# Performance work log

Measured on AMD Instinct MI355X. Metric: run time of the kernel, lower is better.

The kernel has to match this reference:

```python
import jax, jax.numpy as jnp
import numpy as np

B, N, H, E = 16, 512, 8, 128  # batch, nodes, heads, per-head/embed dim
NEG = -1000000000.0


def _xavier(key, shape):
    fan_out, fan_in = shape
    lim = float(np.sqrt(6.0 / (fan_in + fan_out)))
    return jax.random.uniform(key, shape, jnp.float32, -lim, lim)


def setup_inputs() -> dict:
    key = jax.random.key(0)
    ks = jax.random.split(key, 8)
    x = jax.random.normal(ks[0], (B, N, E), jnp.float32)
    dist = jax.random.normal(ks[1], (B, N, N), jnp.float32)
    mask = (jax.random.uniform(ks[2], (B, N)) > 0.2).astype(jnp.float32)
    Wq = _xavier(ks[3], (H * E, E)); bq = jnp.zeros((H * E,), jnp.float32)
    Wk = _xavier(ks[4], (H * E, E)); bk = jnp.zeros((H * E,), jnp.float32)
    Wv = _xavier(ks[5], (H * E, E)); bv = jnp.zeros((H * E,), jnp.float32)
    Wo = _xavier(ks[6], (E, H * E)); bo = jnp.zeros((E,), jnp.float32)
    return dict(x=x, dist=dist, mask=mask, Wq=Wq, bq=bq, Wk=Wk, bk=bk,
                Wv=Wv, bv=bv, Wo=Wo, bo=bo)


def reference(x, dist, mask, Wq, bq, Wk, bk, Wv, bv, Wo, bo):
    b, n, e = x.shape
    h = Wq.shape[0] // e
    scale = e ** (-0.5)
    # projections -> [b, h, n, e]
    q = (x @ Wq.T + bq).reshape(b, n, h, e).transpose(0, 2, 1, 3)
    k = (x @ Wk.T + bk).reshape(b, n, h, e).transpose(0, 2, 1, 3)
    v = (x @ Wv.T + bv).reshape(b, n, h, e).transpose(0, 2, 1, 3)
    # encoder_mask: zero out padded nodes in q, k, v
    m = mask[:, None, :, None]  # [b,1,n,1]
    q = q * m
    k = k * m
    v = v * m
    # scaled scores + per-graph distance bias broadcast over heads
    a = jnp.einsum('bhqe,bhke->bhqk', q * scale, k) + dist[:, None]
    # pairwise attention mask (outer product of node mask)
    am = (mask[:, :, None] * mask[:, None, :])[:, None]  # [b,1,n,n]
    a = jnp.where(am == 0, NEG, a)
    a = jax.nn.softmax(a, axis=-1)
    a = jnp.where(am == 0, 0.0, a)
    # dropout p=0 -> identity
    y = jnp.einsum('bhqk,bhke->bhqe', a, v)
    y = y.transpose(0, 2, 1, 3).reshape(b, n, h * e)
    y = y @ Wo.T + bo
    y = y * mask[:, :, None]
    return y
```

## Files before the change

### kernel.cpp

```cpp
#include <hip/hip_runtime.h>
#include <math.h>

#define BB 16
#define NN 512
#define HH 8
#define EE 128
#define HE 1024
#define QSCALE 0.08838834764831845f
#define NEGV -1000000000.0f

typedef short bf16x8 __attribute__((ext_vector_type(8)));
typedef float f32x4 __attribute__((ext_vector_type(4)));
typedef unsigned u32x4 __attribute__((ext_vector_type(4)));

__device__ __forceinline__ void split2(float v, unsigned short &hi, unsigned short &lo) {
    union { float f; unsigned u; } a; a.f = v;
    const unsigned r = (a.u + 0x7FFFu + ((a.u >> 16) & 1u)) >> 16;
    hi = (unsigned short)r;
    union { unsigned u; float f; } hf; hf.u = r << 16;
    const float res = v - hf.f;
    union { float f; unsigned u; } c; c.f = res;
    const unsigned r2 = (c.u + 0x7FFFu + ((c.u >> 16) & 1u)) >> 16;
    lo = (unsigned short)r2;
}

__device__ __forceinline__ void gload16(const void* g, void* l) {
    __builtin_amdgcn_global_load_lds(
        (const __attribute__((address_space(1))) unsigned*)g,
        (__attribute__((address_space(3))) unsigned*)l, 16, 0, 0);
}

__global__ __launch_bounds__(256) void k_split(
    const float* __restrict__ x,
    const float* __restrict__ Wq, const float* __restrict__ Wk, const float* __restrict__ Wv,
    unsigned short* __restrict__ xhi, unsigned short* __restrict__ xlo,
    unsigned short* __restrict__ wchi, unsigned short* __restrict__ wclo)
{
    const int id = blockIdx.x * 256 + threadIdx.x;
    const int i4 = id * 4;
    const float* src;
    unsigned short *dh, *dl;
    int off;
    if (i4 < 1048576) { src = x; off = i4; dh = xhi + i4; dl = xlo + i4; }
    else {
        const int j = i4 - 1048576;
        const int msel = j >> 17;
        off = j & 131071;
        src = (msel == 0) ? Wq : (msel == 1) ? Wk : Wv;
        dh = wchi + j; dl = wclo + j;
    }
    const float4 v = *reinterpret_cast<const float4*>(src + off);
    unsigned short h[4], l[4];
    split2(v.x, h[0], l[0]); split2(v.y, h[1], l[1]);
    split2(v.z, h[2], l[2]); split2(v.w, h[3], l[3]);
    *reinterpret_cast<ushort4*>(dh) = *reinterpret_cast<ushort4*>(h);
    *reinterpret_cast<ushort4*>(dl) = *reinterpret_cast<ushort4*>(l);
}

__global__ __launch_bounds__(256) void k_split_wo(
    const float* __restrict__ Wo,
    unsigned short* __restrict__ wohi, unsigned short* __restrict__ wolo)
{
    const int i4 = (blockIdx.x * 256 + threadIdx.x) * 4;
    const float4 v = *reinterpret_cast<const float4*>(Wo + i4);
    unsigned short h[4], l[4];
    split2(v.x, h[0], l[0]); split2(v.y, h[1], l[1]);
    split2(v.z, h[2], l[2]); split2(v.w, h[3], l[3]);
    *reinterpret_cast<ushort4*>(wohi + i4) = *reinterpret_cast<ushort4*>(h);
    *reinterpret_cast<ushort4*>(wolo + i4) = *reinterpret_cast<ushort4*>(l);
}

__global__ __launch_bounds__(256, 3) void k_qkv(
    const unsigned short* __restrict__ xhi, const unsigned short* __restrict__ xlo,
    const unsigned short* __restrict__ wchi, const unsigned short* __restrict__ wclo,
    const float* __restrict__ bq, const float* __restrict__ bk, const float* __restrict__ bv,
    unsigned short* __restrict__ Qhi, unsigned short* __restrict__ Qlo,
    unsigned short* __restrict__ Khi, unsigned short* __restrict__ Klo,
    unsigned short* __restrict__ VThi, unsigned short* __restrict__ VTlo)
{
    const int tid = threadIdx.x;
    const int w = tid >> 6, l = tid & 63, g = l >> 4, ln = l & 15;
    const int wm = w >> 1, wc = w & 1;
    const int m0  = blockIdx.x * 128;
    const int c0g = blockIdx.y * 128;
    const int wsel = c0g >> 10;
    const int cc0  = c0g & 1023;
    const float* __restrict__ bias = (wsel == 0) ? bq : (wsel == 1) ? bk : bv;

    f32x4 acc[4][4];
    const f32x4 fz = {0.f, 0.f, 0.f, 0.f};
    #pragma unroll
    for (int i = 0; i < 4; ++i)
        #pragma unroll
        for (int j = 0; j < 4; ++j) acc[i][j] = fz;

    #pragma unroll
    for (int ks = 0; ks < 4; ++ks) {
        bf16x8 ah[4], al[4], bh[4], bl[4];
        #pragma unroll
        for (int i = 0; i < 4; ++i) {
            const size_t a = (size_t)(m0 + wm * 64 + i * 16 + ln) * EE + ks * 32 + g * 8;
            ah[i] = *reinterpret_cast<const bf16x8*>(xhi + a);
            al[i] = *reinterpret_cast<const bf16x8*>(xlo + a);
        }
        #pragma unroll
        for (int j = 0; j < 4; ++j) {
            const size_t a = (size_t)(c0g + wc * 64 + j * 16 + ln) * EE + ks * 32 + g * 8;
            bh[j] = *reinterpret_cast<const bf16x8*>(wchi + a);
            bl[j] = *reinterpret_cast<const bf16x8*>(wclo + a);
        }
        #pragma unroll
        for (int i = 0; i < 4; ++i)
            #pragma unroll
            for (int j = 0; j < 4; ++j) {
                acc[i][j] = __builtin_amdgcn_mfma_f32_16x16x32_bf16(ah[i], bl[j], acc[i][j], 0, 0, 0);
                acc[i][j] = __builtin_amdgcn_mfma_f32_16x16x32_bf16(al[i], bh[j], acc[i][j], 0, 0, 0);
                acc[i][j] = __builtin_amdgcn_mfma_f32_16x16x32_bf16(ah[i], bh[j], acc[i][j], 0, 0, 0);
            }
    }

    const int b  = m0 >> 9;
    const int h  = cc0 >> 7;
    const int bh_ = b * HH + h;
    const int nb = (m0 & (NN - 1));

    if (wsel < 2) {
        unsigned short* __restrict__ hp = (wsel == 0) ? Qhi : Khi;
        unsigned short* __restrict__ lp = (wsel == 0) ? Qlo : Klo;
        #pragma unroll
        for (int j = 0; j < 4; ++j) {
            const int clocal = wc * 64 + j * 16 + ln;
            const float bj = bias[cc0 + clocal];
            #pragma unroll
            for (int i = 0; i < 4; ++i) {
                #pragma unroll
                for (int r = 0; r < 4; ++r) {
                    const int n = nb + wm * 64 + i * 16 + g * 4 + r;
                    unsigned short th, tl;
                    split2(acc[i][j][r] + bj, th, tl);
                    const size_t o = ((size_t)bh_ * NN + n) * EE + clocal;
                    hp[o] = th; lp[o] = tl;
                }
            }
        }
    } else {
        #pragma unroll
        for (int j = 0; j < 4; ++j) {
            const int e = wc * 64 + j * 16 + ln;
            const float bj = bias[cc0 + e];
            #pragma unroll
            for (int i = 0; i < 4; ++i) {
                const int n = nb + wm * 64 + i * 16 + g * 4;
                unsigned short th[4], tl[4];
                #pragma unroll
                for (int r = 0; r < 4; ++r) split2(acc[i][j][r] + bj, th[r], tl[r]);
                const size_t o = ((size_t)bh_ * EE + e) * NN + n;
                *reinterpret_cast<ushort4*>(VThi + o) = *reinterpret_cast<ushort4*>(th);
                *reinterpret_cast<ushort4*>(VTlo + o) = *reinterpret_cast<ushort4*>(tl);
            }
        }
    }
}

__global__ __launch_bounds__(256, 2) void k_attn(
    const unsigned short* __restrict__ Qhi, const unsigned short* __restrict__ Qlo,
    const unsigned short* __restrict__ Khi_g, const unsigned short* __restrict__ Klo_g,
    const unsigned short* __restrict__ VThi_g, const unsigned short* __restrict__ VTlo_g,
    const float* __restrict__ dist, const float* __restrict__ mask,
    unsigned short* __restrict__ Yhi, unsigned short* __restrict__ Ylo)
{
    __shared__ __align__(16) unsigned char smem[65536];
    unsigned short* sKhi = (unsigned short*)smem;
    unsigned short* sKlo = (unsigned short*)(smem + 16384);
    unsigned short* sVhi = (unsigned short*)(smem + 32768);
    unsigned short* sVlo = (unsigned short*)(smem + 49152);
    unsigned* sP = (unsigned*)smem;

    const int tid = threadIdx.x;
    const int w  = tid >> 6;
    const int l  = tid & 63;
    const int g  = l >> 4;
    const int ln = l & 15;
    const int b  = blockIdx.x;
    const int qb = blockIdx.y;
    const int h  = blockIdx.z;
    const int q0 = qb * 128;
    const int bh = b * HH + h;
    const size_t baseQ = (size_t)bh * NN * EE;
    const size_t baseV = (size_t)bh * EE * NN;

    bf16x8 qa_hi[2][4], qa_lo[2][4];
    #pragma unroll
    for (int s = 0; s < 2; ++s)
        #pragma unroll
        for (int ks = 0; ks < 4; ++ks) {
            const size_t qoff = baseQ + (size_t)(q0 + w * 32 + s * 16 + ln) * EE + ks * 32 + g * 8;
            qa_hi[s][ks] = *reinterpret_cast<const bf16x8*>(Qhi + qoff);
            qa_lo[s][ks] = *reinterpret_cast<const bf16x8*>(Qlo + qoff);
        }

    float mq[2][4];
    #pragma unroll
    for (int s = 0; s < 2; ++s)
        #pragma unroll
        for (int r = 0; r < 4; ++r)
            mq[s][r] = mask[b * NN + q0 + w * 32 + s * 16 + g * 4 + r];

    float lrun[2][4];
    f32x4 yacc[2][8];
    const f32x4 fz = {0.f, 0.f, 0.f, 0.f};
    #pragma unroll
    for (int s = 0; s < 2; ++s) {
        #pragma unroll
        for (int r = 0; r < 4; ++r) lrun[s][r] = 0.f;
        #pragma unroll
        for (int et = 0; et < 8; ++et) yacc[s][et] = fz;
    }

    const unsigned short* __restrict__ gK = (w == 0) ? Khi_g : Klo_g;
    const unsigned short* __restrict__ gV = (w == 2) ? VThi_g : VTlo_g;
    unsigned short* sDst = (unsigned short*)(smem + w * 16384);

    for (int kt = 0; kt < 8; ++kt) {
        const int k0 = kt * 64;

        if (w < 2) {
            #pragma unroll
            for (int c = 0; c < 16; ++c) {
                const int n = c * 4 + (l >> 4);
                const int cs = ((l & 15) * 16) ^ ((n & 7) << 4);
                gload16(gK + baseQ + (size_t)(k0 + n) * EE + (cs >> 1),
                        (char*)sDst + c * 1024 + l * 16);
            }
        } else {
            #pragma unroll
            for (int c = 0; c < 16; ++c) {
                const int e = c * 8 + (l >> 3);
                const int cs = ((l & 7) * 16) ^ ((e & 7) << 4);
                gload16(gV + baseV + (size_t)e * NN + k0 + (cs >> 1),
                        (char*)sDst + c * 1024 + l * 16);
            }
        }
        __syncthreads();

        f32x4 sacc[2][4];
        #pragma unroll
        for (int s = 0; s < 2; ++s)
            #pragma unroll
            for (int t = 0; t < 4; ++t) sacc[s][t] = fz;

        __builtin_amdgcn_s_setprio(1);
        #pragma unroll
        for (int ks = 0; ks < 4; ++ks) {
            #pragma unroll
            for (int t = 0; t < 4; ++t) {
                const int row = t * 16 + ln;
                const int off = row * 256 + (((ks * 64) + g * 16) ^ ((row & 7) << 4));
                const bf16x8 kbh = *reinterpret_cast<const bf16x8*>((char*)sKhi + off);
                const bf16x8 kbl = *reinterpret_cast<const bf16x8*>((char*)sKlo + off);
                #pragma unroll
                for (int s = 0; s < 2; ++s) {
                    sacc[s][t] = __builtin_amdgcn_mfma_f32_16x16x32_bf16(qa_hi[s][ks], kbh, sacc[s][t], 0, 0, 0);
                    sacc[s][t] = __builtin_amdgcn_mfma_f32_16x16x32_bf16(qa_lo[s][ks], kbh, sacc[s][t], 0, 0, 0);
                    sacc[s][t] = __builtin_amdgcn_mfma_f32_16x16x32_bf16(qa_hi[s][ks], kbl, sacc[s][t], 0, 0, 0);
                }
            }
        }
        __builtin_amdgcn_s_setprio(0);

        float mk[4];
        #pragma unroll
        for (int t = 0; t < 4; ++t) mk[t] = mask[b * NN + k0 + t * 16 + ln];
        float dv[2][4][4];
        #pragma unroll
        for (int s = 0; s < 2; ++s)
            #pragma unroll
            for (int r = 0; r < 4; ++r) {
                const size_t drow = ((size_t)b * NN + q0 + w * 32 + s * 16 + g * 4 + r) * NN + k0;
                #pragma unroll
                for (int t = 0; t < 4; ++t) dv[s][t][r] = dist[drow + t * 16 + ln];
            }
        __syncthreads();

        #pragma unroll
        for (int s = 0; s < 2; ++s) {
            #pragma unroll
            for (int r = 0; r < 4; ++r) {
                float p[4], ls = 0.f;
                #pragma unroll
                for (int t = 0; t < 4; ++t) {
                    const bool live = (mq[s][r] != 0.f) && (mk[t] != 0.f);
                    const float sv = live ? fmaf(sacc[s][t][r], QSCALE, dv[s][t][r]) : NEGV;
                    p[t] = __expf(sv);
                    ls += p[t];
                }
                lrun[s][r] += ls;
                const int q = w * 32 + s * 16 + g * 4 + r;
                #pragma unroll
                for (int t = 0; t < 4; ++t) {
                    unsigned short ph, pl;
                    split2(p[t], ph, pl);
                    const int k = t * 16 + ln;
                    const int off = q * 256 + ((k * 4) ^ ((q & 7) << 4));
                    *reinterpret_cast<unsigned*>((char*)sP + off) = ((unsigned)ph << 16) | pl;
                }
            }
        }
        __syncthreads();

        __builtin_amdgcn_s_setprio(1);
        #pragma unroll
        for (int ks = 0; ks < 2; ++ks) {
            bf16x8 pah[2], pal[2];
            #pragma unroll
            for (int s = 0; s < 2; ++s) {
                const int q = w * 32 + s * 16 + ln;
                const int swz = (q & 7) << 4;
                const int colb = ks * 128 + g * 32;
                const uint4 r0 = *reinterpret_cast<const uint4*>((char*)sP + q * 256 + (colb ^ swz));
                const uint4 r1 = *reinterpret_cast<const uint4*>((char*)sP + q * 256 + ((colb + 16) ^ swz));
                const unsigned wrd[8] = {r0.x, r0.y, r0.z, r0.w, r1.x, r1.y, r1.z, r1.w};
                unsigned hh[4], llw[4];
                #pragma unroll
                for (int d = 0; d < 4; ++d) {
                    hh[d]  = __builtin_amdgcn_perm(wrd[2 * d + 1], wrd[2 * d], 0x07060302u);
                    llw[d] = __builtin_amdgcn_perm(wrd[2 * d + 1], wrd[2 * d], 0x05040100u);
                }
                u32x4 th = {hh[0], hh[1], hh[2], hh[3]};
                u32x4 tl = {llw[0], llw[1], llw[2], llw[3]};
                pah[s] = __builtin_bit_cast(bf16x8, th);
                pal[s] = __builtin_bit_cast(bf16x8, tl);
            }
            #pragma unroll
            for (int et = 0; et < 8; ++et) {
                const int e = et * 16 + ln;
                const int off = e * 128 + (((ks * 64) + g * 16) ^ ((e & 7) << 4));
                const bf16x8 vbh = *reinterpret_cast<const bf16x8*>((char*)sVhi + off);
                const bf16x8 vbl = *reinterpret_cast<const bf16x8*>((char*)sVlo + off);
                #pragma unroll
                for (int s = 0; s < 2; ++s) {
                    yacc[s][et] = __builtin_amdgcn_mfma_f32_16x16x32_bf16(pah[s], vbh, yacc[s][et], 0, 0, 0);
                    yacc[s][et] = __builtin_amdgcn_mfma_f32_16x16x32_bf16(pal[s], vbh, yacc[s][et], 0, 0, 0);
                    yacc[s][et] = __builtin_amdgcn_mfma_f32_16x16x32_bf16(pah[s], vbl, yacc[s][et], 0, 0, 0);
                }
            }
        }
        __builtin_amdgcn_s_setprio(0);
        __syncthreads();
    }

    #pragma unroll
    for (int s = 0; s < 2; ++s) {
        float inv[4];
        #pragma unroll
        for (int r = 0; r < 4; ++r) {
            float ls = lrun[s][r];
            ls += __shfl_xor(ls, 1);
            ls += __shfl_xor(ls, 2);
            ls += __shfl_xor(ls, 4);
            ls += __shfl_xor(ls, 8);
            inv[r] = 1.0f / fmaxf(ls, 1e-30f);
        }
        #pragma unroll
        for (int et = 0; et < 8; ++et) {
            #pragma unroll
            for (int r = 0; r < 4; ++r) {
                const int q = q0 + w * 32 + s * 16 + g * 4 + r;
                const size_t o = ((size_t)(b * NN + q)) * HE + h * EE + et * 16 + ln;
                unsigned short th, tl;
                split2(yacc[s][et][r] * inv[r], th, tl);
                Yhi[o] = th; Ylo[o] = tl;
            }
        }
    }
}

__global__ __launch_bounds__(256) void k_out(
    const unsigned short* __restrict__ Yhi, const unsigned short* __restrict__ Ylo,
    const unsigned short* __restrict__ wohi, const unsigned short* __restrict__ wolo,
    const float* __restrict__ bo, const float* __restrict__ mask,
    float* __restrict__ out)
{
    const int tid = threadIdx.x;
    const int w = tid >> 6, l = tid & 63, g = l >> 4, ln = l & 15;
    const int m0 = blockIdx.x * 16;
    const int cq = w * 32;

    f32x4 acc[2];
    const f32x4 fz = {0.f, 0.f, 0.f, 0.f};
    acc[0] = fz; acc[1] = fz;

    #pragma unroll 4
    for (int ks = 0; ks < 32; ++ks) {
        const size_t a = (size_t)(m0 + ln) * HE + ks * 32 + g * 8;
        const bf16x8 ah = *reinterpret_cast<const bf16x8*>(Yhi + a);
        const bf16x8 al = *reinterpret_cast<const bf16x8*>(Ylo + a);
        #pragma unroll
        for (int jc = 0; jc < 2; ++jc) {
            const size_t bo_ = (size_t)(cq + jc * 16 + ln) * HE + ks * 32 + g * 8;
            const bf16x8 bh = *reinterpret_cast<const bf16x8*>(wohi + bo_);
            const bf16x8 bl = *reinterpret_cast<const bf16x8*>(wolo + bo_);
            acc[jc] = __builtin_amdgcn_mfma_f32_16x16x32_bf16(ah, bl, acc[jc], 0, 0, 0);
            acc[jc] = __builtin_amdgcn_mfma_f32_16x16x32_bf16(al, bh, acc[jc], 0, 0, 0);
            acc[jc] = __builtin_amdgcn_mfma_f32_16x16x32_bf16(ah, bh, acc[jc], 0, 0, 0);
        }
    }

    #pragma unroll
    for (int jc = 0; jc < 2; ++jc) {
        const int c = cq + jc * 16 + ln;
        const float bc = bo[c];
        #pragma unroll
        for (int r = 0; r < 4; ++r) {
            const int m = m0 + g * 4 + r;
            const int b = m >> 9, n = m & (NN - 1);
            out[(size_t)m * EE + c] = (acc[jc][r] + bc) * mask[b * NN + n];
        }
    }
}

extern "C" void kernel_launch(void* const* d_in, const int* in_sizes, int n_in,
                              void* d_out, int out_size, void* d_ws, size_t ws_size,
                              hipStream_t stream) {
    const float* x    = (const float*)d_in[0];
    const float* dist = (const float*)d_in[1];
    const float* mask = (const float*)d_in[2];
    const float* Wq   = (const float*)d_in[3];
    const float* bq   = (const float*)d_in[4];
    const float* Wk   = (const float*)d_in[5];
    const float* bk   = (const float*)d_in[6];
    const float* Wv   = (const float*)d_in[7];
    const float* bv   = (const float*)d_in[8];
    const float* Wo   = (const float*)d_in[9];
    const float* bo   = (const float*)d_in[10];
    float* out = (float*)d_out;

    const size_t SZ = (size_t)BB * HH * NN * EE;
    if (ws_size < SZ * 16) return;
    char* ws = (char*)d_ws;
    unsigned short* Qhi  = (unsigned short*)(ws);
    unsigned short* Qlo  = (unsigned short*)(ws + 1 * 16777216);
    unsigned short* Khi  = (unsigned short*)(ws + 2 * 16777216);
    unsigned short* Klo  = (unsigned short*)(ws + 3 * 16777216);
    unsigned short* VThi = (unsigned short*)(ws + 4 * 16777216);
    unsigned short* VTlo = (unsigned short*)(ws + 5 * 16777216);
    char* yreg = ws + 6 * 16777216;
    unsigned short* Yhi  = (unsigned short*)(yreg);
    unsigned short* Ylo  = (unsigned short*)(yreg + 16777216);
    unsigned short* xhi  = (unsigned short*)(yreg);
    unsigned short* xlo  = (unsigned short*)(yreg + 2097152);
    unsigned short* wchi = (unsigned short*)(yreg + 4194304);
    unsigned short* wclo = (unsigned short*)(yreg + 4980736);
    unsigned short* wohi = (unsigned short*)(ws);
    unsigned short* wolo = (unsigned short*)(ws + 262144);

    k_split<<<1408, 256, 0, stream>>>(x, Wq, Wk, Wv, xhi, xlo, wchi, wclo);
    k_qkv<<<dim3(64, 24), 256, 0, stream>>>(xhi, xlo, wchi, wclo, bq, bk, bv,
                                            Qhi, Qlo, Khi, Klo, VThi, VTlo);
    k_attn<<<dim3(BB, NN / 128, HH), 256, 0, stream>>>(Qhi, Qlo, Khi, Klo, VThi, VTlo,
                                                       dist, mask, Yhi, Ylo);
    k_split_wo<<<128, 256, 0, stream>>>(Wo, wohi, wolo);
    k_out<<<512, 256, 0, stream>>>(Yhi, Ylo, wohi, wolo, bo, mask, out);
}
```

Measured before the change: 314.0 us.

## Load K/V directly from global in attention, halve query tile, vectorize epilogue stores

The attention kernel no longer stages K and V through LDS with async global-to-LDS loads. Each wave now reads K and V fragments straight from global memory, and each block handles 64 queries (16 per wave) instead of 128, which doubles the grid and cuts LDS use to the P buffer. The QKV, attention and output GEMMs swap MFMA operand order so each lane holds four consecutive columns, which turns the scalar epilogue stores into ushort4/float4 vector stores. The risk is higher global/L2 traffic, since K/V are re-read per wave and per block without LDS sharing.

```diff
diff --git a/kernel.cpp b/kernel.cpp
--- a/kernel.cpp
+++ b/kernel.cpp
@@ -22,12 +22,6 @@
     union { float f; unsigned u; } c; c.f = res;
     const unsigned r2 = (c.u + 0x7FFFu + ((c.u >> 16) & 1u)) >> 16;
     lo = (unsigned short)r2;
-}
-
-__device__ __forceinline__ void gload16(const void* g, void* l) {
-    __builtin_amdgcn_global_load_lds(
-        (const __attribute__((address_space(1))) unsigned*)g,
-        (__attribute__((address_space(3))) unsigned*)l, 16, 0, 0);
 }
 
 __global__ __launch_bounds__(256) void k_split(
@@ -109,14 +103,25 @@
             bh[j] = *reinterpret_cast<const bf16x8*>(wchi + a);
             bl[j] = *reinterpret_cast<const bf16x8*>(wclo + a);
         }
-        #pragma unroll
-        for (int i = 0; i < 4; ++i)
-            #pragma unroll
-            for (int j = 0; j < 4; ++j) {
-                acc[i][j] = __builtin_amdgcn_mfma_f32_16x16x32_bf16(ah[i], bl[j], acc[i][j], 0, 0, 0);
-                acc[i][j] = __builtin_amdgcn_mfma_f32_16x16x32_bf16(al[i], bh[j], acc[i][j], 0, 0, 0);
-                acc[i][j] = __builtin_amdgcn_mfma_f32_16x16x32_bf16(ah[i], bh[j], acc[i][j], 0, 0, 0);
-            }
+        if (wsel < 2) {
+            #pragma unroll
+            for (int j = 0; j < 4; ++j)
+                #pragma unroll
+                for (int i = 0; i < 4; ++i) {
+                    acc[j][i] = __builtin_amdgcn_mfma_f32_16x16x32_bf16(bh[j], al[i], acc[j][i], 0, 0, 0);
+                    acc[j][i] = __builtin_amdgcn_mfma_f32_16x16x32_bf16(bl[j], ah[i], acc[j][i], 0, 0, 0);
+                    acc[j][i] = __builtin_amdgcn_mfma_f32_16x16x32_bf16(bh[j], ah[i], acc[j][i], 0, 0, 0);
+                }
+        } else {
+            #pragma unroll
+            for (int i = 0; i < 4; ++i)
+                #pragma unroll
+                for (int j = 0; j < 4; ++j) {
+                    acc[i][j] = __builtin_amdgcn_mfma_f32_16x16x32_bf16(ah[i], bl[j], acc[i][j], 0, 0, 0);
+                    acc[i][j] = __builtin_amdgcn_mfma_f32_16x16x32_bf16(al[i], bh[j], acc[i][j], 0, 0, 0);
+                    acc[i][j] = __builtin_amdgcn_mfma_f32_16x16x32_bf16(ah[i], bh[j], acc[i][j], 0, 0, 0);
+                }
+        }
     }
 
     const int b  = m0 >> 9;
@@ -129,18 +134,18 @@
         unsigned short* __restrict__ lp = (wsel == 0) ? Qlo : Klo;
         #pragma unroll
         for (int j = 0; j < 4; ++j) {
-            const int clocal = wc * 64 + j * 16 + ln;
-            const float bj = bias[cc0 + clocal];
+            const int e0 = wc * 64 + j * 16 + g * 4;
+            const float4 b4 = *reinterpret_cast<const float4*>(bias + cc0 + e0);
+            const float bb4[4] = {b4.x, b4.y, b4.z, b4.w};
             #pragma unroll
             for (int i = 0; i < 4; ++i) {
+                const int n = nb + wm * 64 + i * 16 + ln;
+                unsigned short th[4], tl[4];
                 #pragma unroll
-                for (int r = 0; r < 4; ++r) {
-                    const int n = nb + wm * 64 + i * 16 + g * 4 + r;
-                    unsigned short th, tl;
-                    split2(acc[i][j][r] + bj, th, tl);
-                    const size_t o = ((size_t)bh_ * NN + n) * EE + clocal;
-                    hp[o] = th; lp[o] = tl;
-                }
+                for (int r = 0; r < 4; ++r) split2(acc[j][i][r] + bb4[r], th[r], tl[r]);
+                const size_t o = ((size_t)bh_ * NN + n) * EE + e0;
+                *reinterpret_cast<ushort4*>(hp + o) = *reinterpret_cast<ushort4*>(th);
+                *reinterpret_cast<ushort4*>(lp + o) = *reinterpret_cast<ushort4*>(tl);
             }
         }
     } else {
@@ -169,12 +174,8 @@
     const float* __restrict__ dist, const float* __restrict__ mask,
     unsigned short* __restrict__ Yhi, unsigned short* __restrict__ Ylo)
 {
-    __shared__ __align__(16) unsigned char smem[65536];
-    unsigned short* sKhi = (unsigned short*)smem;
-    unsigned short* sKlo = (unsigned short*)(smem + 16384);
-    unsigned short* sVhi = (unsigned short*)(smem + 32768);
-    unsigned short* sVlo = (unsigned short*)(smem + 49152);
-    unsigned* sP = (unsigned*)smem;
+    __shared__ __align__(16) unsigned sP[64 * 64];
+    __shared__ float sL[64];
 
     const int tid = threadIdx.x;
     const int w  = tid >> 6;
@@ -184,194 +185,136 @@
     const int b  = blockIdx.x;
     const int qb = blockIdx.y;
     const int h  = blockIdx.z;
-    const int q0 = qb * 128;
+    const int q0 = qb * 64;
     const int bh = b * HH + h;
     const size_t baseQ = (size_t)bh * NN * EE;
     const size_t baseV = (size_t)bh * EE * NN;
 
-    bf16x8 qa_hi[2][4], qa_lo[2][4];
-    #pragma unroll
-    for (int s = 0; s < 2; ++s)
-        #pragma unroll
-        for (int ks = 0; ks < 4; ++ks) {
-            const size_t qoff = baseQ + (size_t)(q0 + w * 32 + s * 16 + ln) * EE + ks * 32 + g * 8;
-            qa_hi[s][ks] = *reinterpret_cast<const bf16x8*>(Qhi + qoff);
-            qa_lo[s][ks] = *reinterpret_cast<const bf16x8*>(Qlo + qoff);
-        }
-
-    float mq[2][4];
-    #pragma unroll
-    for (int s = 0; s < 2; ++s)
-        #pragma unroll
-        for (int r = 0; r < 4; ++r)
-            mq[s][r] = mask[b * NN + q0 + w * 32 + s * 16 + g * 4 + r];
-
-    float lrun[2][4];
-    f32x4 yacc[2][8];
+    bf16x8 qa_hi[4], qa_lo[4];
+    #pragma unroll
+    for (int ks = 0; ks < 4; ++ks) {
+        const size_t qoff = baseQ + (size_t)(q0 + w * 16 + ln) * EE + ks * 32 + g * 8;
+        qa_hi[ks] = *reinterpret_cast<const bf16x8*>(Qhi + qoff);
+        qa_lo[ks] = *reinterpret_cast<const bf16x8*>(Qlo + qoff);
+    }
+
+    float mq[4];
+    #pragma unroll
+    for (int r = 0; r < 4; ++r) mq[r] = mask[b * NN + q0 + w * 16 + g * 4 + r];
+
+    float lrun[4] = {0.f, 0.f, 0.f, 0.f};
+    f32x4 yacc[8];
     const f32x4 fz = {0.f, 0.f, 0.f, 0.f};
     #pragma unroll
-    for (int s = 0; s < 2; ++s) {
-        #pragma unroll
-        for (int r = 0; r < 4; ++r) lrun[s][r] = 0.f;
-        #pragma unroll
-        for (int et = 0; et < 8; ++et) yacc[s][et] = fz;
-    }
-
-    const unsigned short* __restrict__ gK = (w == 0) ? Khi_g : Klo_g;
-    const unsigned short* __restrict__ gV = (w == 2) ? VThi_g : VTlo_g;
-    unsigned short* sDst = (unsigned short*)(smem + w * 16384);
+    for (int et = 0; et < 8; ++et) yacc[et] = fz;
 
     for (int kt = 0; kt < 8; ++kt) {
         const int k0 = kt * 64;
 
-        if (w < 2) {
-            #pragma unroll
-            for (int c = 0; c < 16; ++c) {
-                const int n = c * 4 + (l >> 4);
-                const int cs = ((l & 15) * 16) ^ ((n & 7) << 4);
-                gload16(gK + baseQ + (size_t)(k0 + n) * EE + (cs >> 1),
-                        (char*)sDst + c * 1024 + l * 16);
-            }
-        } else {
-            #pragma unroll
-            for (int c = 0; c < 16; ++c) {
-                const int e = c * 8 + (l >> 3);
-                const int cs = ((l & 7) * 16) ^ ((e & 7) << 4);
-                gload16(gV + baseV + (size_t)e * NN + k0 + (cs >> 1),
-                        (char*)sDst + c * 1024 + l * 16);
+        f32x4 sacc[4];
+        #pragma unroll
+        for (int t = 0; t < 4; ++t) sacc[t] = fz;
+
+        #pragma unroll
+        for (int ks = 0; ks < 4; ++ks) {
+            #pragma unroll
+            for (int t = 0; t < 4; ++t) {
+                const size_t ko = baseQ + (size_t)(k0 + t * 16 + ln) * EE + ks * 32 + g * 8;
+                const bf16x8 kbh = *reinterpret_cast<const bf16x8*>(Khi_g + ko);
+                const bf16x8 kbl = *reinterpret_cast<const bf16x8*>(Klo_g + ko);
+                sacc[t] = __builtin_amdgcn_mfma_f32_16x16x32_bf16(qa_hi[ks], kbh, sacc[t], 0, 0, 0);
+                sacc[t] = __builtin_amdgcn_mfma_f32_16x16x32_bf16(qa_lo[ks], kbh, sacc[t], 0, 0, 0);
+                sacc[t] = __builtin_amdgcn_mfma_f32_16x16x32_bf16(qa_hi[ks], kbl, sacc[t], 0, 0, 0);
+            }
+        }
+
+        float mk[4];
+        #pragma unroll
+        for (int t = 0; t < 4; ++t) mk[t] = mask[b * NN + k0 + t * 16 + ln];
+        float dv[4][4];
+        #pragma unroll
+        for (int r = 0; r < 4; ++r) {
+            const size_t drow = ((size_t)b * NN + q0 + w * 16 + g * 4 + r) * NN + k0;
+            #pragma unroll
+            for (int t = 0; t < 4; ++t) dv[t][r] = dist[drow + t * 16 + ln];
+        }
+
+        #pragma unroll
+        for (int r = 0; r < 4; ++r) {
+            float p[4], ls = 0.f;
+            #pragma unroll
+            for (int t = 0; t < 4; ++t) {
+                const bool live = (mq[r] != 0.f) && (mk[t] != 0.f);
+                const float sv = live ? fmaf(sacc[t][r], QSCALE, dv[t][r]) : NEGV;
+                p[t] = __expf(sv);
+                ls += p[t];
+            }
+            lrun[r] += ls;
+            const int q = w * 16 + g * 4 + r;
+            #pragma unroll
+            for (int t = 0; t < 4; ++t) {
+                unsigned short ph, pl;
+                split2(p[t], ph, pl);
+                const int k = t * 16 + ln;
+                const int off = q * 256 + ((k * 4) ^ ((q & 7) << 4));
+                *reinterpret_cast<unsigned*>((char*)sP + off) = ((unsigned)ph << 16) | pl;
             }
         }
         __syncthreads();
 
-        f32x4 sacc[2][4];
-        #pragma unroll
-        for (int s = 0; s < 2; ++s)
-            #pragma unroll
-            for (int t = 0; t < 4; ++t) sacc[s][t] = fz;
-
-        __builtin_amdgcn_s_setprio(1);
-        #pragma unroll
-        for (int ks = 0; ks < 4; ++ks) {
-            #pragma unroll
-            for (int t = 0; t < 4; ++t) {
-                const int row = t * 16 + ln;
-                const int off = row * 256 + (((ks * 64) + g * 16) ^ ((row & 7) << 4));
-                const bf16x8 kbh = *reinterpret_cast<const bf16x8*>((char*)sKhi + off);
-                const bf16x8 kbl = *reinterpret_cast<const bf16x8*>((char*)sKlo + off);
-                #pragma unroll
-                for (int s = 0; s < 2; ++s) {
-                    sacc[s][t] = __builtin_amdgcn_mfma_f32_16x16x32_bf16(qa_hi[s][ks], kbh, sacc[s][t], 0, 0, 0);
-                    sacc[s][t] = __builtin_amdgcn_mfma_f32_16x16x32_bf16(qa_lo[s][ks], kbh, sacc[s][t], 0, 0, 0);
-                    sacc[s][t] = __builtin_amdgcn_mfma_f32_16x16x32_bf16(qa_hi[s][ks], kbl, sacc[s][t], 0, 0, 0);
-                }
-            }
-        }
-        __builtin_amdgcn_s_setprio(0);
-
-        float mk[4];
-        #pragma unroll
-        for (int t = 0; t < 4; ++t) mk[t] = mask[b * NN + k0 + t * 16 + ln];
-        float dv[2][4][4];
-        #pragma unroll
-        for (int s = 0; s < 2; ++s)
-            #pragma unroll
-            for (int r = 0; r < 4; ++r) {
-                const size_t drow = ((size_t)b * NN + q0 + w * 32 + s * 16 + g * 4 + r) * NN + k0;
-                #pragma unroll
-                for (int t = 0; t < 4; ++t) dv[s][t][r] = dist[drow + t * 16 + ln];
-            }
+        #pragma unroll
+        for (int ks = 0; ks < 2; ++ks) {
+            const int q = w * 16 + ln;
+            const int swz = (q & 7) << 4;
+            const int colb = ks * 128 + g * 32;
+            const uint4 r0 = *reinterpret_cast<const uint4*>((char*)sP + q * 256 + (colb ^ swz));
+            const uint4 r1 = *reinterpret_cast<const uint4*>((char*)sP + q * 256 + ((colb + 16) ^ swz));
+            const unsigned wrd[8] = {r0.x, r0.y, r0.z, r0.w, r1.x, r1.y, r1.z, r1.w};
+            unsigned hh[4], llw[4];
+            #pragma unroll
+            for (int d = 0; d < 4; ++d) {
+                hh[d]  = __builtin_amdgcn_perm(wrd[2 * d + 1], wrd[2 * d], 0x07060302u);
+                llw[d] = __builtin_amdgcn_perm(wrd[2 * d + 1], wrd[2 * d], 0x05040100u);
+            }
+            u32x4 th = {hh[0], hh[1], hh[2], hh[3]};
+            u32x4 tl = {llw[0], llw[1], llw[2], llw[3]};
+            const bf16x8 pah = __builtin_bit_cast(bf16x8, th);
+            const bf16x8 pal = __builtin_bit_cast(bf16x8, tl);
+
+            #pragma unroll
+            for (int et = 0; et < 8; ++et) {
+                const size_t vo = baseV + (size_t)(et * 16 + ln) * NN + k0 + ks * 32 + g * 8;
+                const bf16x8 vbh = *reinterpret_cast<const bf16x8*>(VThi_g + vo);
+                const bf16x8 vbl = *reinterpret_cast<const bf16x8*>(VTlo_g + vo);
+                yacc[et] = __builtin_amdgcn_mfma_f32_16x16x32_bf16(vbh, pal, yacc[et], 0, 0, 0);
+                yacc[et] = __builtin_amdgcn_mfma_f32_16x16x32_bf16(vbl, pah, yacc[et], 0, 0, 0);
+                yacc[et] = __builtin_amdgcn_mfma_f32_16x16x32_bf16(vbh, pah, yacc[et], 0, 0, 0);
+            }
+        }
         __syncthreads();
-
-        #pragma unroll
-        for (int s = 0; s < 2; ++s) {
-            #pragma unroll
-            for (int r = 0; r < 4; ++r) {
-                float p[4], ls = 0.f;
-                #pragma unroll
-                for (int t = 0; t < 4; ++t) {
-                    const bool live = (mq[s][r] != 0.f) && (mk[t] != 0.f);
-                    const float sv = live ? fmaf(sacc[s][t][r], QSCALE, dv[s][t][r]) : NEGV;
-                    p[t] = __expf(sv);
-                    ls += p[t];
-                }
-                lrun[s][r] += ls;
-                const int q = w * 32 + s * 16 + g * 4 + r;
-                #pragma unroll
-                for (int t = 0; t < 4; ++t) {
-                    unsigned short ph, pl;
-                    split2(p[t], ph, pl);
-                    const int k = t * 16 + ln;
-                    const int off = q * 256 + ((k * 4) ^ ((q & 7) << 4));
-                    *reinterpret_cast<unsigned*>((char*)sP + off) = ((unsigned)ph << 16) | pl;
-                }
-            }
-        }
-        __syncthreads();
-
-        __builtin_amdgcn_s_setprio(1);
-        #pragma unroll
-        for (int ks = 0; ks < 2; ++ks) {
-            bf16x8 pah[2], pal[2];
-            #pragma unroll
-            for (int s = 0; s < 2; ++s) {
-                const int q = w * 32 + s * 16 + ln;
-                const int swz = (q & 7) << 4;
-                const int colb = ks * 128 + g * 32;
-                const uint4 r0 = *reinterpret_cast<const uint4*>((char*)sP + q * 256 + (colb ^ swz));
-                const uint4 r1 = *reinterpret_cast<const uint4*>((char*)sP + q * 256 + ((colb + 16) ^ swz));
-                const unsigned wrd[8] = {r0.x, r0.y, r0.z, r0.w, r1.x, r1.y, r1.z, r1.w};
-                unsigned hh[4], llw[4];
-                #pragma unroll
-                for (int d = 0; d < 4; ++d) {
-                    hh[d]  = __builtin_amdgcn_perm(wrd[2 * d + 1], wrd[2 * d], 0x07060302u);
-                    llw[d] = __builtin_amdgcn_perm(wrd[2 * d + 1], wrd[2 * d], 0x05040100u);
-                }
-                u32x4 th = {hh[0], hh[1], hh[2], hh[3]};
-                u32x4 tl = {llw[0], llw[1], llw[2], llw[3]};
-                pah[s] = __builtin_bit_cast(bf16x8, th);
-                pal[s] = __builtin_bit_cast(bf16x8, tl);
-            }
-            #pragma unroll
-            for (int et = 0; et < 8; ++et) {
-                const int e = et * 16 + ln;
-                const int off = e * 128 + (((ks * 64) + g * 16) ^ ((e & 7) << 4));
-                const bf16x8 vbh = *reinterpret_cast<const bf16x8*>((char*)sVhi + off);
-                const bf16x8 vbl = *reinterpret_cast<const bf16x8*>((char*)sVlo + off);
-                #pragma unroll
-                for (int s = 0; s < 2; ++s) {
-                    yacc[s][et] = __builtin_amdgcn_mfma_f32_16x16x32_bf16(pah[s], vbh, yacc[s][et], 0, 0, 0);
-                    yacc[s][et] = __builtin_amdgcn_mfma_f32_16x16x32_bf16(pal[s], vbh, yacc[s][et], 0, 0, 0);
-                    yacc[s][et] = __builtin_amdgcn_mfma_f32_16x16x32_bf16(pah[s], vbl, yacc[s][et], 0, 0, 0);
-                }
-            }
-        }
-        __builtin_amdgcn_s_setprio(0);
-        __syncthreads();
-    }
-
-    #pragma unroll
-    for (int s = 0; s < 2; ++s) {
-        float inv[4];
-        #pragma unroll
-        for (int r = 0; r < 4; ++r) {
-            float ls = lrun[s][r];
-            ls += __shfl_xor(ls, 1);
-            ls += __shfl_xor(ls, 2);
-            ls += __shfl_xor(ls, 4);
-            ls += __shfl_xor(ls, 8);
-            inv[r] = 1.0f / fmaxf(ls, 1e-30f);
-        }
-        #pragma unroll
-        for (int et = 0; et < 8; ++et) {
-            #pragma unroll
-            for (int r = 0; r < 4; ++r) {
-                const int q = q0 + w * 32 + s * 16 + g * 4 + r;
-                const size_t o = ((size_t)(b * NN + q)) * HE + h * EE + et * 16 + ln;
-                unsigned short th, tl;
-                split2(yacc[s][et][r] * inv[r], th, tl);
-                Yhi[o] = th; Ylo[o] = tl;
-            }
-        }
+    }
+
+    #pragma unroll
+    for (int r = 0; r < 4; ++r) {
+        float ls = lrun[r];
+        ls += __shfl_xor(ls, 1);
+        ls += __shfl_xor(ls, 2);
+        ls += __shfl_xor(ls, 4);
+        ls += __shfl_xor(ls, 8);
+        sL[w * 16 + g * 4 + r] = ls;
+    }
+    __syncthreads();
+    const float linv = 1.0f / fmaxf(sL[w * 16 + ln], 1e-30f);
+
+    const int q = q0 + w * 16 + ln;
+    #pragma unroll
+    for (int et = 0; et < 8; ++et) {
+        unsigned short th[4], tl[4];
+        #pragma unroll
+        for (int r = 0; r < 4; ++r) split2(yacc[et][r] * linv, th[r], tl[r]);
+        const size_t o = ((size_t)(b * NN + q)) * HE + h * EE + et * 16 + g * 4;
+        *reinterpret_cast<ushort4*>(Yhi + o) = *reinterpret_cast<ushort4*>(th);
+        *reinterpret_cast<ushort4*>(Ylo + o) = *reinterpret_cast<ushort4*>(tl);
     }
 }
 
@@ -400,22 +343,25 @@
             const size_t bo_ = (size_t)(cq + jc * 16 + ln) * HE + ks * 32 + g * 8;
             const bf16x8 bh = *reinterpret_cast<const bf16x8*>(wohi + bo_);
             const bf16x8 bl = *reinterpret_cast<const bf16x8*>(wolo + bo_);
-            acc[jc] = __builtin_amdgcn_mfma_f32_16x16x32_bf16(ah, bl, acc[jc], 0, 0, 0);
-            acc[jc] = __builtin_amdgcn_mfma_f32_16x16x32_bf16(al, bh, acc[jc], 0, 0, 0);
-            acc[jc] = __builtin_amdgcn_mfma_f32_16x16x32_bf16(ah, bh, acc[jc], 0, 0, 0);
-        }
-    }
-
+            acc[jc] = __builtin_amdgcn_mfma_f32_16x16x32_bf16(bh, al, acc[jc], 0, 0, 0);
+            acc[jc] = __builtin_amdgcn_mfma_f32_16x16x32_bf16(bl, ah, acc[jc], 0, 0, 0);
+            acc[jc] = __builtin_amdgcn_mfma_f32_16x16x32_bf16(bh, ah, acc[jc], 0, 0, 0);
+        }
+    }
+
+    const int m = m0 + ln;
+    const int b = m >> 9, n = m & (NN - 1);
+    const float mm = mask[b * NN + n];
     #pragma unroll
     for (int jc = 0; jc < 2; ++jc) {
-        const int c = cq + jc * 16 + ln;
-        const float bc = bo[c];
-        #pragma unroll
-        for (int r = 0; r < 4; ++r) {
-            const int m = m0 + g * 4 + r;
-            const int b = m >> 9, n = m & (NN - 1);
-            out[(size_t)m * EE + c] = (acc[jc][r] + bc) * mask[b * NN + n];
-        }
+        const int c0 = cq + jc * 16 + g * 4;
+        const float4 b4 = *reinterpret_cast<const float4*>(bo + c0);
+        float4 o;
+        o.x = (acc[jc][0] + b4.x) * mm;
+        o.y = (acc[jc][1] + b4.y) * mm;
+        o.z = (acc[jc][2] + b4.z) * mm;
+        o.w = (acc[jc][3] + b4.w) * mm;
+        *reinterpret_cast<float4*>(out + (size_t)m * EE + c0) = o;
     }
 }
 
@@ -457,8 +403,8 @@
     k_split<<<1408, 256, 0, stream>>>(x, Wq, Wk, Wv, xhi, xlo, wchi, wclo);
     k_qkv<<<dim3(64, 24), 256, 0, stream>>>(xhi, xlo, wchi, wclo, bq, bk, bv,
                                             Qhi, Qlo, Khi, Klo, VThi, VTlo);
-    k_attn<<<dim3(BB, NN / 128, HH), 256, 0, stream>>>(Qhi, Qlo, Khi, Klo, VThi, VTlo,
-                                                       dist, mask, Yhi, Ylo);
+    k_attn<<<dim3(BB, NN / 64, HH), 256, 0, stream>>>(Qhi, Qlo, Khi, Klo, VThi, VTlo,
+                                                      dist, mask, Yhi, Ylo);
     k_split_wo<<<128, 256, 0, stream>>>(Wo, wohi, wolo);
     k_out<<<512, 256, 0, stream>>>(Yhi, Ylo, wohi, wolo, bo, mask, out);
 }
```

After: 552.3 us. 75.9% more time.
